# Kernel tuning notes

Hardware: AMD Instinct MI355X
Metric: run time of the kernel (lower is better)

The kernel has to match this reference:

```python
import jax, jax.numpy as jnp
import numpy as np

B, S, H, NH, HD, L, BASE = 2, 2048, 2048, 16, 128, 512, 10000.0
ROT = H // 2  # rotary embedding dim = 1024


def _linear_params(key, out_dim, in_dim, scale=0.02):
    kw, kb = jax.random.split(key)
    W = jax.random.normal(kw, (out_dim, in_dim), dtype=jnp.float32) * scale
    b = jax.random.normal(kb, (out_dim,), dtype=jnp.float32) * scale
    return W, b


def setup_inputs() -> dict:
    key = jax.random.key(0)
    ks = jax.random.split(key, 8)
    Wq_down, bq_down = _linear_params(ks[0], L, H)
    Wkv_down, bkv_down = _linear_params(ks[1], L, H)
    Wq_up, bq_up = _linear_params(ks[2], H, L)
    Wk_nope, bk_nope = _linear_params(ks[3], H // 2, L)
    Wk_rope, bk_rope = _linear_params(ks[4], H // 2, L)
    Wv_up, bv_up = _linear_params(ks[5], H, L)
    Wo, bo = _linear_params(ks[6], H, H)
    hidden_states = jax.random.normal(ks[7], (B, S, H), dtype=jnp.float32)
    return {
        "hidden_states": hidden_states,
        "Wq_down": Wq_down, "bq_down": bq_down,
        "Wkv_down": Wkv_down, "bkv_down": bkv_down,
        "Wq_up": Wq_up, "bq_up": bq_up,
        "Wk_nope": Wk_nope, "bk_nope": bk_nope,
        "Wk_rope": Wk_rope, "bk_rope": bk_rope,
        "Wv_up": Wv_up, "bv_up": bv_up,
        "Wo": Wo, "bo": bo,
    }


def _rope_cache(seq_len):
    inv_freq = 1.0 / (BASE ** (jnp.arange(0, ROT, 2, dtype=jnp.float32) / ROT))
    t = jnp.arange(seq_len, dtype=jnp.float32)
    freqs = jnp.outer(t, inv_freq)                      # [S, ROT/2]
    emb = jnp.concatenate([freqs, freqs], axis=-1)      # [S, ROT]
    return jnp.cos(emb)[:, :ROT], jnp.sin(emb)[:, :ROT]


def _apply_rotary(x, cos, sin):
    half = x.shape[-1] // 2
    x1, x2 = x[..., :half], x[..., half:]
    c, s = cos[..., :half], sin[..., :half]
    return jnp.concatenate([x1 * c - x2 * s, x1 * s + x2 * c], axis=-1)


def reference(hidden_states, Wq_down, bq_down, Wkv_down, bkv_down,
              Wq_up, bq_up, Wk_nope, bk_nope, Wk_rope, bk_rope,
              Wv_up, bv_up, Wo, bo):
    bsz, seq_len, _ = hidden_states.shape
    lin = lambda x, W, b: x @ W.T + b

    q_latent = lin(hidden_states, Wq_down, bq_down)     # [B,S,L]
    kv_latent = lin(hidden_states, Wkv_down, bkv_down)  # [B,S,L]

    q = lin(q_latent, Wq_up, bq_up)                     # [B,S,H]
    k_nope = lin(kv_latent, Wk_nope, bk_nope)           # [B,S,H/2]
    cos, sin = _rope_cache(seq_len)
    k_rope = _apply_rotary(lin(kv_latent, Wk_rope, bk_rope), cos, sin)  # [B,S,H/2]
    k = jnp.concatenate([k_nope, k_rope], axis=-1)      # [B,S,H]
    v = lin(kv_latent, Wv_up, bv_up)                    # [B,S,H]

    def split_heads(x):
        return x.reshape(bsz, seq_len, NH, HD).transpose(0, 2, 1, 3)  # [B,NH,S,HD]

    qh, kh, vh = split_heads(q), split_heads(k), split_heads(v)
    scale = 1.0 / np.sqrt(HD).astype(np.float32)
    scores = jnp.einsum('bhqd,bhkd->bhqk', qh, kh) * scale  # [B,NH,S,S]
    attn = jax.nn.softmax(scores, axis=-1)  # dropout p=0 -> identity
    out = jnp.einsum('bhqk,bhkd->bhqd', attn, vh)           # [B,NH,S,HD]
    out = out.transpose(0, 2, 1, 3).reshape(bsz, seq_len, H)
    return lin(out, Wo, bo)
```

## Files before the change

### kernel.cpp

```cpp
#include <hip/hip_runtime.h>
#include <math.h>

#define B_  2
#define S_  2048
#define H_  2048
#define NH_ 16
#define HD_ 128

typedef __attribute__((ext_vector_type(8))) short short8;
typedef __attribute__((ext_vector_type(4))) float f32x4;

#define AS1 __attribute__((address_space(1)))
#define AS3 __attribute__((address_space(3)))

#define QSCALE_LOG2 (0.08838834764831845f * 1.4426950408889634f)

__device__ __forceinline__ ushort f2bf(float f) {
    union { float f; unsigned u; } x; x.f = f;
    unsigned r = (x.u + 0x7FFF + ((x.u >> 16) & 1)) >> 16;
    return (ushort)r;
}
__device__ __forceinline__ float bf2f(ushort u) {
    union { unsigned u; float f; } x; x.u = ((unsigned)u) << 16;
    return x.f;
}
__device__ __forceinline__ void gload_lds16(const void* g, void* l) {
    __builtin_amdgcn_global_load_lds((const AS1 void*)g, (AS3 void*)l, 16, 0, 0);
}

struct CastSeg { const float* src; ushort* dst; unsigned n4; };
struct CastParams { CastSeg seg[8]; unsigned total4; };

__global__ __launch_bounds__(256)
void cast_all(CastParams p)
{
    unsigned i = blockIdx.x * 256 + threadIdx.x;
    if (i >= p.total4) return;
#pragma unroll
    for (int s = 0; s < 8; ++s) {
        if (i < p.seg[s].n4) {
            const float4 v = reinterpret_cast<const float4*>(p.seg[s].src)[i];
            ushort4 o;
            o.x = f2bf(v.x); o.y = f2bf(v.y); o.z = f2bf(v.z); o.w = f2bf(v.w);
            reinterpret_cast<ushort4*>(p.seg[s].dst)[i] = o;
            return;
        }
        i -= p.seg[s].n4;
    }
}

__global__ __launch_bounds__(256)
void gemm_down(const ushort* __restrict__ hs,
               const ushort* __restrict__ wqd, const ushort* __restrict__ wkvd,
               const float* __restrict__ bqd, const float* __restrict__ bkvd,
               ushort* __restrict__ latq, ushort* __restrict__ latkv)
{
    constexpr int K = 2048;
    __shared__ ushort Asm[128 * 32];
    __shared__ ushort Bsm[64 * 32];

    const int tid  = threadIdx.x;
    const int w    = tid >> 6;
    const int lane = tid & 63;
    const int lo   = lane & 15;
    const int hi   = lane >> 4;
    const int m0   = blockIdx.y * 128;
    const int n0   = blockIdx.x * 64;
    const int l4   = lane >> 2;
    const int s4   = lane & 3;

    const int seg = n0 >> 9;
    const int nl  = n0 & 511;
    const ushort* W    = (seg ? wkvd : wqd) + (size_t)nl * K;
    const float*  bias = (seg ? bkvd : bqd) + nl;
    ushort*       outp = seg ? latkv : latq;

    f32x4 acc[2][4];
#pragma unroll
    for (int i = 0; i < 2; ++i)
#pragma unroll
        for (int j = 0; j < 4; ++j) acc[i][j] = f32x4{0.f, 0.f, 0.f, 0.f};

    for (int k0 = 0; k0 < K; k0 += 32) {
        __syncthreads();
#pragma unroll
        for (int t = 0; t < 2; ++t) {
            const int row = w * 32 + t * 16 + l4;
            gload_lds16(hs + (size_t)(m0 + row) * K + k0 + s4 * 8,
                        (char*)Asm + w * 2048 + t * 1024);
        }
        {
            const int row = w * 16 + l4;
            gload_lds16(W + (size_t)row * K + k0 + s4 * 8,
                        (char*)Bsm + w * 1024);
        }
        __syncthreads();

        short8 a[2], b[4];
#pragma unroll
        for (int i = 0; i < 2; ++i)
            a[i] = *reinterpret_cast<const short8*>(&Asm[(w * 32 + i * 16 + lo) * 32 + hi * 8]);
#pragma unroll
        for (int j = 0; j < 4; ++j)
            b[j] = *reinterpret_cast<const short8*>(&Bsm[(j * 16 + lo) * 32 + hi * 8]);
#pragma unroll
        for (int i = 0; i < 2; ++i)
#pragma unroll
            for (int j = 0; j < 4; ++j)
                acc[i][j] = __builtin_amdgcn_mfma_f32_16x16x32_bf16(a[i], b[j], acc[i][j], 0, 0, 0);
    }

#pragma unroll
    for (int j = 0; j < 4; ++j) {
        const int col = j * 16 + lo;
        const float bv = bias[col];
#pragma unroll
        for (int i = 0; i < 2; ++i) {
            const int row0 = m0 + w * 32 + i * 16 + hi * 4;
#pragma unroll
            for (int r = 0; r < 4; ++r)
                outp[(size_t)(row0 + r) * 512 + nl + col] = f2bf(acc[i][j][r] + bv);
        }
    }
}

__global__ __launch_bounds__(256)
void gemm_up(const ushort* __restrict__ latq, const ushort* __restrict__ latkv,
             const ushort* __restrict__ wqu, const ushort* __restrict__ wkn,
             const ushort* __restrict__ wkr, const ushort* __restrict__ wvu,
             const float* __restrict__ bq, const float* __restrict__ bkn,
             const float* __restrict__ bkr, const float* __restrict__ bv,
             ushort* __restrict__ qb, ushort* __restrict__ kb,
             ushort* __restrict__ krp, ushort* __restrict__ vt)
{
    constexpr int K = 512;
    __shared__ ushort Asm[128 * 32];
    __shared__ ushort Bsm[128 * 32];

    const int tid  = threadIdx.x;
    const int w    = tid >> 6;
    const int lane = tid & 63;
    const int lo   = lane & 15;
    const int hi   = lane >> 4;
    const int wm   = w >> 1;
    const int wn   = w & 1;
    const int m0   = blockIdx.y * 128;
    const int n0   = blockIdx.x * 128;
    const int l4   = lane >> 2;
    const int s4   = lane & 3;

    const ushort* A;  const ushort* W;  const float* bias;
    ushort* outp = nullptr;  int ldc = 0;  int ncol0;  int mode;
    if (n0 < 2048)      { A = latq;  W = wqu + (size_t)n0 * K;          bias = bq  + n0;
                          outp = qb;  ldc = 2048; ncol0 = n0;        mode = 2; }
    else if (n0 < 3072) { A = latkv; W = wkn + (size_t)(n0 - 2048) * K; bias = bkn + (n0 - 2048);
                          outp = kb;  ldc = 2048; ncol0 = n0 - 2048; mode = 1; }
    else if (n0 < 4096) { A = latkv; W = wkr + (size_t)(n0 - 3072) * K; bias = bkr + (n0 - 3072);
                          outp = krp; ldc = 1024; ncol0 = n0 - 3072; mode = 1; }
    else                { A = latkv; W = wvu + (size_t)(n0 - 4096) * K; bias = bv  + (n0 - 4096);
                          outp = vt;  ldc = 0;    ncol0 = n0 - 4096; mode = 3; }

    f32x4 acc[4][4];
#pragma unroll
    for (int i = 0; i < 4; ++i)
#pragma unroll
        for (int j = 0; j < 4; ++j) acc[i][j] = f32x4{0.f, 0.f, 0.f, 0.f};

    for (int k0 = 0; k0 < K; k0 += 32) {
        __syncthreads();
#pragma unroll
        for (int t = 0; t < 2; ++t) {
            const int row = w * 32 + t * 16 + l4;
            gload_lds16(A + (size_t)(m0 + row) * K + k0 + s4 * 8,
                        (char*)Asm + w * 2048 + t * 1024);
            gload_lds16(W + (size_t)row * K + k0 + s4 * 8,
                        (char*)Bsm + w * 2048 + t * 1024);
        }
        __syncthreads();

        short8 a[4], b[4];
#pragma unroll
        for (int i = 0; i < 4; ++i)
            a[i] = *reinterpret_cast<const short8*>(&Asm[(wm * 64 + i * 16 + lo) * 32 + hi * 8]);
#pragma unroll
        for (int j = 0; j < 4; ++j)
            b[j] = *reinterpret_cast<const short8*>(&Bsm[(wn * 64 + j * 16 + lo) * 32 + hi * 8]);
#pragma unroll
        for (int i = 0; i < 4; ++i)
#pragma unroll
            for (int j = 0; j < 4; ++j)
                acc[i][j] = __builtin_amdgcn_mfma_f32_16x16x32_bf16(a[i], b[j], acc[i][j], 0, 0, 0);
    }

#pragma unroll
    for (int j = 0; j < 4; ++j) {
        const int col = wn * 64 + j * 16 + lo;
        const float bb = bias[col];
#pragma unroll
        for (int i = 0; i < 4; ++i) {
            const int row0 = m0 + wm * 64 + i * 16 + hi * 4;
            if (mode == 3) {
                const int gcol = ncol0 + col;
                const int hh = gcol >> 7, dd = gcol & 127;
                const int bbi = row0 >> 11, sidx = row0 & 2047;
                ushort4 o;
                o.x = f2bf(acc[i][j][0] + bb);
                o.y = f2bf(acc[i][j][1] + bb);
                o.z = f2bf(acc[i][j][2] + bb);
                o.w = f2bf(acc[i][j][3] + bb);
                *reinterpret_cast<ushort4*>(
                    vt + (((size_t)(bbi * 16 + hh) * 128 + dd) << 11) + sidx) = o;
            } else if (mode == 2) {
#pragma unroll
                for (int r = 0; r < 4; ++r)
                    outp[(size_t)(row0 + r) * ldc + ncol0 + col] =
                        f2bf((acc[i][j][r] + bb) * QSCALE_LOG2);
            } else {
#pragma unroll
                for (int r = 0; r < 4; ++r)
                    outp[(size_t)(row0 + r) * ldc + ncol0 + col] =
                        f2bf(acc[i][j][r] + bb);
            }
        }
    }
}

__global__ __launch_bounds__(256)
void gemm_out(const ushort* __restrict__ A, const ushort* __restrict__ W,
              const float* __restrict__ bias, float* __restrict__ C)
{
    constexpr int K = 2048;
    __shared__ ushort Asm[128 * 32];
    __shared__ ushort Bsm[128 * 32];

    const int tid  = threadIdx.x;
    const int w    = tid >> 6;
    const int lane = tid & 63;
    const int lo   = lane & 15;
    const int hi   = lane >> 4;
    const int wm   = w >> 1;
    const int wn   = w & 1;
    const int m0   = blockIdx.y * 128;
    const int n0   = blockIdx.x * 128;
    const int l4   = lane >> 2;
    const int s4   = lane & 3;

    f32x4 acc[4][4];
#pragma unroll
    for (int i = 0; i < 4; ++i)
#pragma unroll
        for (int j = 0; j < 4; ++j) acc[i][j] = f32x4{0.f, 0.f, 0.f, 0.f};

    for (int k0 = 0; k0 < K; k0 += 32) {
        __syncthreads();
#pragma unroll
        for (int t = 0; t < 2; ++t) {
            const int row = w * 32 + t * 16 + l4;
            gload_lds16(A + (size_t)(m0 + row) * K + k0 + s4 * 8,
                        (char*)Asm + w * 2048 + t * 1024);
            gload_lds16(W + (size_t)(n0 + row) * K + k0 + s4 * 8,
                        (char*)Bsm + w * 2048 + t * 1024);
        }
        __syncthreads();

        short8 a[4], b[4];
#pragma unroll
        for (int i = 0; i < 4; ++i)
            a[i] = *reinterpret_cast<const short8*>(&Asm[(wm * 64 + i * 16 + lo) * 32 + hi * 8]);
#pragma unroll
        for (int j = 0; j < 4; ++j)
            b[j] = *reinterpret_cast<const short8*>(&Bsm[(wn * 64 + j * 16 + lo) * 32 + hi * 8]);
#pragma unroll
        for (int i = 0; i < 4; ++i)
#pragma unroll
            for (int j = 0; j < 4; ++j)
                acc[i][j] = __builtin_amdgcn_mfma_f32_16x16x32_bf16(a[i], b[j], acc[i][j], 0, 0, 0);
    }

#pragma unroll
    for (int j = 0; j < 4; ++j) {
        const int col = n0 + wn * 64 + j * 16 + lo;
        const float bb = bias[col];
#pragma unroll
        for (int i = 0; i < 4; ++i) {
            const int row0 = m0 + wm * 64 + i * 16 + hi * 4;
#pragma unroll
            for (int r = 0; r < 4; ++r)
                C[(size_t)(row0 + r) * 2048 + col] = acc[i][j][r] + bb;
        }
    }
}

__global__ void rope_bf(const ushort* __restrict__ pre, ushort* __restrict__ kb)
{
    const int row = blockIdx.x;
    const int d   = blockIdx.y * 256 + threadIdx.x;
    const int pos = row & (S_ - 1);
    const float inv = expf((float)d * -0.017988946f);
    const float ang = (float)pos * inv;
    const float c = cosf(ang), s = sinf(ang);
    const float x1 = bf2f(pre[(size_t)row * 1024 + d]);
    const float x2 = bf2f(pre[(size_t)row * 1024 + 512 + d]);
    kb[(size_t)row * 2048 + 1024 + d]       = f2bf(x1 * c - x2 * s);
    kb[(size_t)row * 2048 + 1024 + 512 + d] = f2bf(x1 * s + x2 * c);
}

__global__ __launch_bounds__(512)
void attn_mfma(const ushort* __restrict__ Q, const ushort* __restrict__ K,
               const ushort* __restrict__ Vt, ushort* __restrict__ O)
{
    __shared__ ushort Kl[64 * 128];
    __shared__ ushort Vl[128 * 72];
    __shared__ ushort Pl[8 * 16 * 72];

    const int tid  = threadIdx.x;
    const int w    = tid >> 6;
    const int lane = tid & 63;
    const int lo   = lane & 15;
    const int hi   = lane >> 4;
    const int bh   = blockIdx.y;
    const int b    = bh >> 4;
    const int q0   = blockIdx.x * 128;
    const size_t headoff = (size_t)(bh & 15) * HD_;

    short8 aq[4];
    {
        const ushort* qrow = Q + (size_t)(b * S_ + q0 + w * 16 + lo) * H_ + headoff;
#pragma unroll
        for (int kd = 0; kd < 4; ++kd)
            aq[kd] = *reinterpret_cast<const short8*>(qrow + kd * 32 + hi * 8);
    }

    f32x4 oacc[8];
#pragma unroll
    for (int fd = 0; fd < 8; ++fd) oacc[fd] = f32x4{0.f, 0.f, 0.f, 0.f};
    float m_run[4], l_run[4];
#pragma unroll
    for (int r = 0; r < 4; ++r) { m_run[r] = -INFINITY; l_run[r] = 0.f; }

    const ushort* kbase = K  + (size_t)(b * S_) * H_ + headoff;
    const ushort* vbase = Vt + (size_t)bh * 128 * S_;

    short8 kst[2], vst[2];
    auto issue_loads = [&](int kt) {
#pragma unroll
        for (int r = 0; r < 2; ++r) {
            const int c = r * 512 + tid;
            kst[r] = *reinterpret_cast<const short8*>(
                kbase + (size_t)(kt * 64 + (c >> 4)) * H_ + (c & 15) * 8);
            vst[r] = *reinterpret_cast<const short8*>(
                vbase + (size_t)(c >> 3) * S_ + kt * 64 + (c & 7) * 8);
        }
    };
    auto write_lds = [&]() {
#pragma unroll
        for (int r = 0; r < 2; ++r) {
            const int c = r * 512 + tid;
            const int key = c >> 4, slot = c & 15;
            *reinterpret_cast<short8*>(
                (char*)Kl + key * 256 + ((slot * 16) ^ ((key & 7) << 4))) = kst[r];
            *reinterpret_cast<short8*>(
                (char*)Vl + (c >> 3) * 144 + (c & 7) * 16) = vst[r];
        }
    };

    issue_loads(0);
    write_lds();
    __syncthreads();

    const int swz = (lo & 7) << 4;

    for (int kt = 0; kt < S_ / 64; ++kt) {
        if (kt + 1 < S_ / 64) issue_loads(kt + 1);

        f32x4 s[4];
#pragma unroll
        for (int fn = 0; fn < 4; ++fn) s[fn] = f32x4{0.f, 0.f, 0.f, 0.f};

        __builtin_amdgcn_s_setprio(1);
#pragma unroll
        for (int fn = 0; fn < 4; ++fn) {
            const int kbyte = (fn * 16 + lo) * 256;
#pragma unroll
            for (int kd = 0; kd < 4; ++kd) {
                short8 bk = *reinterpret_cast<const short8*>(
                    (const char*)Kl + kbyte + ((kd * 64 + hi * 16) ^ swz));
                s[fn] = __builtin_amdgcn_mfma_f32_16x16x32_bf16(aq[kd], bk, s[fn], 0, 0, 0);
            }
        }
        __builtin_amdgcn_s_setprio(0);

        float f_r[4];
        bool resc = false;
#pragma unroll
        for (int r = 0; r < 4; ++r) {
            const float s0 = s[0][r], s1 = s[1][r], s2 = s[2][r], s3 = s[3][r];
            float mx = fmaxf(fmaxf(s0, s1), fmaxf(s2, s3));
            mx = fmaxf(mx, __shfl_xor(mx, 1));
            mx = fmaxf(mx, __shfl_xor(mx, 2));
            mx = fmaxf(mx, __shfl_xor(mx, 4));
            mx = fmaxf(mx, __shfl_xor(mx, 8));
            if (mx - m_run[r] > 8.0f) {
                f_r[r] = exp2f(m_run[r] - mx);
                m_run[r] = mx;
                resc = true;
            } else {
                f_r[r] = 1.0f;
            }
            const float p0 = exp2f(s0 - m_run[r]), p1 = exp2f(s1 - m_run[r]),
                        p2 = exp2f(s2 - m_run[r]), p3 = exp2f(s3 - m_run[r]);
            float ls = p0 + p1 + p2 + p3;
            ls += __shfl_xor(ls, 1);
            ls += __shfl_xor(ls, 2);
            ls += __shfl_xor(ls, 4);
            ls += __shfl_xor(ls, 8);
            l_run[r] = l_run[r] * f_r[r] + ls;
            ushort* prow = &Pl[(size_t)(w * 16 + hi * 4 + r) * 72 + lo];
            prow[0]  = f2bf(p0);
            prow[16] = f2bf(p1);
            prow[32] = f2bf(p2);
            prow[48] = f2bf(p3);
        }

        if (__any((int)resc)) {
#pragma unroll
            for (int fd = 0; fd < 8; ++fd)
#pragma unroll
                for (int r = 0; r < 4; ++r)
                    oacc[fd][r] *= f_r[r];
        }

        __builtin_amdgcn_s_setprio(1);
#pragma unroll
        for (int ks = 0; ks < 2; ++ks) {
            short8 pa = *reinterpret_cast<const short8*>(
                (const char*)Pl + (w * 16 + lo) * 144 + ks * 64 + hi * 16);
#pragma unroll
            for (int fd = 0; fd < 8; ++fd) {
                short8 bv = *reinterpret_cast<const short8*>(
                    (const char*)Vl + (fd * 16 + lo) * 144 + ks * 64 + hi * 16);
                oacc[fd] = __builtin_amdgcn_mfma_f32_16x16x32_bf16(pa, bv, oacc[fd], 0, 0, 0);
            }
        }
        __builtin_amdgcn_s_setprio(0);

        __syncthreads();
        if (kt + 1 < S_ / 64) {
            write_lds();
            __syncthreads();
        }
    }

#pragma unroll
    for (int r = 0; r < 4; ++r) {
        const float inv = 1.0f / l_run[r];
        ushort* orow = O + (size_t)(b * S_ + q0 + w * 16 + hi * 4 + r) * H_
                         + headoff + lo;
#pragma unroll
        for (int fd = 0; fd < 8; ++fd)
            orow[fd * 16] = f2bf(oacc[fd][r] * inv);
    }
}

extern "C" void kernel_launch(void* const* d_in, const int* in_sizes, int n_in,
                              void* d_out, int out_size, void* d_ws, size_t ws_size,
                              hipStream_t stream)
{
    const float* hs       = (const float*)d_in[0];
    const float* Wq_down  = (const float*)d_in[1];
    const float* bq_down  = (const float*)d_in[2];
    const float* Wkv_down = (const float*)d_in[3];
    const float* bkv_down = (const float*)d_in[4];
    const float* Wq_up    = (const float*)d_in[5];
    const float* bq_up    = (const float*)d_in[6];
    const float* Wk_nope  = (const float*)d_in[7];
    const float* bk_nope  = (const float*)d_in[8];
    const float* Wk_rope  = (const float*)d_in[9];
    const float* bk_rope  = (const float*)d_in[10];
    const float* Wv_up    = (const float*)d_in[11];
    const float* bv_up    = (const float*)d_in[12];
    const float* Wo       = (const float*)d_in[13];
    const float* bo       = (const float*)d_in[14];
    float* out = (float*)d_out;

    ushort* ws = (ushort*)d_ws;
    ushort* hs_bf   = ws;
    ushort* wqd_bf  = hs_bf  + (size_t)8388608;
    ushort* wkvd_bf = wqd_bf + (size_t)1048576;
    ushort* wqu_bf  = wkvd_bf+ (size_t)1048576;
    ushort* wkn_bf  = wqu_bf + (size_t)1048576;
    ushort* wkr_bf  = wkn_bf + (size_t)524288;
    ushort* wvu_bf  = wkr_bf + (size_t)524288;
    ushort* wo_bf   = wvu_bf + (size_t)1048576;
    ushort* lat_q   = wo_bf  + (size_t)4194304;
    ushort* lat_kv  = lat_q  + (size_t)2097152;
    ushort* qb      = lat_kv + (size_t)2097152;
    ushort* kb      = qb     + (size_t)8388608;
    ushort* krp     = kb     + (size_t)8388608;
    ushort* vt      = krp    + (size_t)4194304;
    ushort* ob      = vt     + (size_t)8388608;

    const int M = B_ * S_;

    CastParams cp;
    cp.seg[0] = { hs,       hs_bf,   8388608u / 4 };
    cp.seg[1] = { Wq_down,  wqd_bf,  1048576u / 4 };
    cp.seg[2] = { Wkv_down, wkvd_bf, 1048576u / 4 };
    cp.seg[3] = { Wq_up,    wqu_bf,  1048576u / 4 };
    cp.seg[4] = { Wk_nope,  wkn_bf,   524288u / 4 };
    cp.seg[5] = { Wk_rope,  wkr_bf,   524288u / 4 };
    cp.seg[6] = { Wv_up,    wvu_bf,  1048576u / 4 };
    cp.seg[7] = { Wo,       wo_bf,   4194304u / 4 };
    cp.total4 = (8388608u + 1048576u * 4 + 524288u * 2 + 4194304u) / 4;
    cast_all<<<(cp.total4 + 255) / 256, 256, 0, stream>>>(cp);

    gemm_down<<<dim3(16, 32), 256, 0, stream>>>(
        hs_bf, wqd_bf, wkvd_bf, bq_down, bkv_down, lat_q, lat_kv);

    gemm_up<<<dim3(48, 32), 256, 0, stream>>>(
        lat_q, lat_kv, wqu_bf, wkn_bf, wkr_bf, wvu_bf,
        bq_up, bk_nope, bk_rope, bv_up, qb, kb, krp, vt);

    rope_bf<<<dim3(M, 2), 256, 0, stream>>>(krp, kb);

    attn_mfma<<<dim3(S_ / 128, B_ * NH_), 512, 0, stream>>>(qb, kb, vt, ob);

    gemm_out<<<dim3(16, 32), 256, 0, stream>>>(ob, wo_bf, bo, out);
}
```

Measured before the change: 410.7 us.

## Transpose attention score MFMA for per-lane softmax rows; shrink output GEMM tile

The QK^T MFMA now swaps its operands so each lane holds one query row's scores across its accumulators. Row max and sum therefore need only two cross-lane shuffles instead of four per row. P is written to LDS as packed bf16 via v_cvt_pk_bf16_f32 in 8-byte stores, and rescale factors and l are fetched with __shfl where they are needed. Separately, the output projection GEMM uses 128x64 tiles with a 1D warp layout, doubling the grid to 32x32 blocks to improve occupancy and CU fill, at the cost of more A-tile reloads.

```diff
diff --git a/kernel.cpp b/kernel.cpp
--- a/kernel.cpp
+++ b/kernel.cpp
@@ -23,6 +23,11 @@
 __device__ __forceinline__ float bf2f(ushort u) {
     union { unsigned u; float f; } x; x.u = ((unsigned)u) << 16;
     return x.f;
+}
+__device__ __forceinline__ unsigned cvt_pk_bf16(float a, float b) {
+    unsigned r;
+    asm("v_cvt_pk_bf16_f32 %0, %1, %2" : "=v"(r) : "v"(a), "v"(b));
+    return r;
 }
 __device__ __forceinline__ void gload_lds16(const void* g, void* l) {
     __builtin_amdgcn_global_load_lds((const AS1 void*)g, (AS3 void*)l, 16, 0, 0);
@@ -231,23 +236,21 @@
 {
     constexpr int K = 2048;
     __shared__ ushort Asm[128 * 32];
-    __shared__ ushort Bsm[128 * 32];
+    __shared__ ushort Bsm[64 * 32];
 
     const int tid  = threadIdx.x;
     const int w    = tid >> 6;
     const int lane = tid & 63;
     const int lo   = lane & 15;
     const int hi   = lane >> 4;
-    const int wm   = w >> 1;
-    const int wn   = w & 1;
     const int m0   = blockIdx.y * 128;
-    const int n0   = blockIdx.x * 128;
+    const int n0   = blockIdx.x * 64;
     const int l4   = lane >> 2;
     const int s4   = lane & 3;
 
-    f32x4 acc[4][4];
-#pragma unroll
-    for (int i = 0; i < 4; ++i)
+    f32x4 acc[2][4];
+#pragma unroll
+    for (int i = 0; i < 2; ++i)
 #pragma unroll
         for (int j = 0; j < 4; ++j) acc[i][j] = f32x4{0.f, 0.f, 0.f, 0.f};
 
@@ -258,20 +261,23 @@
             const int row = w * 32 + t * 16 + l4;
             gload_lds16(A + (size_t)(m0 + row) * K + k0 + s4 * 8,
                         (char*)Asm + w * 2048 + t * 1024);
+        }
+        {
+            const int row = w * 16 + l4;
             gload_lds16(W + (size_t)(n0 + row) * K + k0 + s4 * 8,
-                        (char*)Bsm + w * 2048 + t * 1024);
-        }
-        __syncthreads();
-
-        short8 a[4], b[4];
-#pragma unroll
-        for (int i = 0; i < 4; ++i)
-            a[i] = *reinterpret_cast<const short8*>(&Asm[(wm * 64 + i * 16 + lo) * 32 + hi * 8]);
+                        (char*)Bsm + w * 1024);
+        }
+        __syncthreads();
+
+        short8 a[2], b[4];
+#pragma unroll
+        for (int i = 0; i < 2; ++i)
+            a[i] = *reinterpret_cast<const short8*>(&Asm[(w * 32 + i * 16 + lo) * 32 + hi * 8]);
 #pragma unroll
         for (int j = 0; j < 4; ++j)
-            b[j] = *reinterpret_cast<const short8*>(&Bsm[(wn * 64 + j * 16 + lo) * 32 + hi * 8]);
-#pragma unroll
-        for (int i = 0; i < 4; ++i)
+            b[j] = *reinterpret_cast<const short8*>(&Bsm[(j * 16 + lo) * 32 + hi * 8]);
+#pragma unroll
+        for (int i = 0; i < 2; ++i)
 #pragma unroll
             for (int j = 0; j < 4; ++j)
                 acc[i][j] = __builtin_amdgcn_mfma_f32_16x16x32_bf16(a[i], b[j], acc[i][j], 0, 0, 0);
@@ -279,11 +285,11 @@
 
 #pragma unroll
     for (int j = 0; j < 4; ++j) {
-        const int col = n0 + wn * 64 + j * 16 + lo;
+        const int col = n0 + j * 16 + lo;
         const float bb = bias[col];
 #pragma unroll
-        for (int i = 0; i < 4; ++i) {
-            const int row0 = m0 + wm * 64 + i * 16 + hi * 4;
+        for (int i = 0; i < 2; ++i) {
+            const int row0 = m0 + w * 32 + i * 16 + hi * 4;
 #pragma unroll
             for (int r = 0; r < 4; ++r)
                 C[(size_t)(row0 + r) * 2048 + col] = acc[i][j][r] + bb;
@@ -334,9 +340,7 @@
     f32x4 oacc[8];
 #pragma unroll
     for (int fd = 0; fd < 8; ++fd) oacc[fd] = f32x4{0.f, 0.f, 0.f, 0.f};
-    float m_run[4], l_run[4];
-#pragma unroll
-    for (int r = 0; r < 4; ++r) { m_run[r] = -INFINITY; l_run[r] = 0.f; }
+    float m_run = -INFINITY, l_run = 0.f;
 
     const ushort* kbase = K  + (size_t)(b * S_) * H_ + headoff;
     const ushort* vbase = Vt + (size_t)bh * 128 * S_;
@@ -373,9 +377,9 @@
     for (int kt = 0; kt < S_ / 64; ++kt) {
         if (kt + 1 < S_ / 64) issue_loads(kt + 1);
 
-        f32x4 s[4];
-#pragma unroll
-        for (int fn = 0; fn < 4; ++fn) s[fn] = f32x4{0.f, 0.f, 0.f, 0.f};
+        f32x4 st[4];
+#pragma unroll
+        for (int fn = 0; fn < 4; ++fn) st[fn] = f32x4{0.f, 0.f, 0.f, 0.f};
 
         __builtin_amdgcn_s_setprio(1);
 #pragma unroll
@@ -385,49 +389,58 @@
             for (int kd = 0; kd < 4; ++kd) {
                 short8 bk = *reinterpret_cast<const short8*>(
                     (const char*)Kl + kbyte + ((kd * 64 + hi * 16) ^ swz));
-                s[fn] = __builtin_amdgcn_mfma_f32_16x16x32_bf16(aq[kd], bk, s[fn], 0, 0, 0);
+                st[fn] = __builtin_amdgcn_mfma_f32_16x16x32_bf16(bk, aq[kd], st[fn], 0, 0, 0);
             }
         }
         __builtin_amdgcn_s_setprio(0);
 
-        float f_r[4];
+        float mx = st[0][0];
+#pragma unroll
+        for (int fn = 0; fn < 4; ++fn)
+#pragma unroll
+            for (int r = 0; r < 4; ++r) mx = fmaxf(mx, st[fn][r]);
+        mx = fmaxf(mx, __shfl_xor(mx, 16));
+        mx = fmaxf(mx, __shfl_xor(mx, 32));
+
+        float fscale = 1.0f;
         bool resc = false;
-#pragma unroll
-        for (int r = 0; r < 4; ++r) {
-            const float s0 = s[0][r], s1 = s[1][r], s2 = s[2][r], s3 = s[3][r];
-            float mx = fmaxf(fmaxf(s0, s1), fmaxf(s2, s3));
-            mx = fmaxf(mx, __shfl_xor(mx, 1));
-            mx = fmaxf(mx, __shfl_xor(mx, 2));
-            mx = fmaxf(mx, __shfl_xor(mx, 4));
-            mx = fmaxf(mx, __shfl_xor(mx, 8));
-            if (mx - m_run[r] > 8.0f) {
-                f_r[r] = exp2f(m_run[r] - mx);
-                m_run[r] = mx;
-                resc = true;
-            } else {
-                f_r[r] = 1.0f;
+        if (mx > m_run + 8.0f) {
+            fscale = exp2f(m_run - mx);
+            m_run = mx;
+            resc = true;
+        }
+
+        float p[4][4];
+        float ls = 0.f;
+#pragma unroll
+        for (int fn = 0; fn < 4; ++fn)
+#pragma unroll
+            for (int r = 0; r < 4; ++r) {
+                p[fn][r] = exp2f(st[fn][r] - m_run);
+                ls += p[fn][r];
             }
-            const float p0 = exp2f(s0 - m_run[r]), p1 = exp2f(s1 - m_run[r]),
-                        p2 = exp2f(s2 - m_run[r]), p3 = exp2f(s3 - m_run[r]);
-            float ls = p0 + p1 + p2 + p3;
-            ls += __shfl_xor(ls, 1);
-            ls += __shfl_xor(ls, 2);
-            ls += __shfl_xor(ls, 4);
-            ls += __shfl_xor(ls, 8);
-            l_run[r] = l_run[r] * f_r[r] + ls;
-            ushort* prow = &Pl[(size_t)(w * 16 + hi * 4 + r) * 72 + lo];
-            prow[0]  = f2bf(p0);
-            prow[16] = f2bf(p1);
-            prow[32] = f2bf(p2);
-            prow[48] = f2bf(p3);
+        ls += __shfl_xor(ls, 16);
+        ls += __shfl_xor(ls, 32);
+        l_run = l_run * fscale + ls;
+
+        {
+            char* prow = (char*)Pl + (w * 16 + lo) * 144 + hi * 8;
+#pragma unroll
+            for (int fn = 0; fn < 4; ++fn) {
+                uint2 u;
+                u.x = cvt_pk_bf16(p[fn][0], p[fn][1]);
+                u.y = cvt_pk_bf16(p[fn][2], p[fn][3]);
+                *reinterpret_cast<uint2*>(prow + fn * 32) = u;
+            }
         }
 
         if (__any((int)resc)) {
 #pragma unroll
-            for (int fd = 0; fd < 8; ++fd)
-#pragma unroll
-                for (int r = 0; r < 4; ++r)
-                    oacc[fd][r] *= f_r[r];
+            for (int r = 0; r < 4; ++r) {
+                const float fr = __shfl(fscale, hi * 4 + r);
+#pragma unroll
+                for (int fd = 0; fd < 8; ++fd) oacc[fd][r] *= fr;
+            }
         }
 
         __builtin_amdgcn_s_setprio(1);
@@ -453,7 +466,8 @@
 
 #pragma unroll
     for (int r = 0; r < 4; ++r) {
-        const float inv = 1.0f / l_run[r];
+        const float lr  = __shfl(l_run, hi * 4 + r);
+        const float inv = 1.0f / lr;
         ushort* orow = O + (size_t)(b * S_ + q0 + w * 16 + hi * 4 + r) * H_
                          + headoff + lo;
 #pragma unroll
@@ -525,5 +539,5 @@
 
     attn_mfma<<<dim3(S_ / 128, B_ * NH_), 512, 0, stream>>>(qb, kb, vt, ob);
 
-    gemm_out<<<dim3(16, 32), 256, 0, stream>>>(ob, wo_bf, bo, out);
-}
+    gemm_out<<<dim3(32, 32), 256, 0, stream>>>(ob, wo_bf, bo, out);
+}
```

Result: faster. 380.5 us (-7.4%).
